# Performance work log

Hardware: AMD Instinct MI355X
Metric: run time of the kernel (lower is better)

Reference implementation:

```python
import jax, jax.numpy as jnp
import numpy as np

N_NODES = 100000
N_EDGES = 1600000
D_IN = 256
D_OUT = 128


def setup_inputs() -> dict:
    key = jax.random.key(0)
    k1, k2, k3, k4, k5, k6 = jax.random.split(key, 6)
    inp = {
        "input": jax.random.normal(k1, (N_NODES, D_IN), dtype=jnp.float32),
        "edge_row": jax.random.randint(k2, (N_EDGES,), 0, N_NODES),
        "edge_col": jax.random.randint(k3, (N_EDGES,), 0, N_NODES),
        "edge_val": jax.random.uniform(k4, (N_EDGES,), dtype=jnp.float32),
        "W": jax.random.normal(k5, (D_IN, D_OUT), dtype=jnp.float32) * (1.0 / np.sqrt(D_IN)),
        "b": jax.random.normal(k6, (D_OUT,), dtype=jnp.float32) * 0.01,
    }
    return inp


def reference(input, edge_row, edge_col, edge_val, W, b):
    # support = Linear(input)  -> [N, D_OUT]
    support = jnp.dot(input, W) + b
    # sparse.mm(adj, support): out[r] = sum_e val[e] * support[col[e]] for edges with row[e]==r
    msgs = edge_val[:, None] * support[edge_col]  # [E, D_OUT]
    agg = jax.ops.segment_sum(msgs, edge_row, num_segments=N_NODES)  # [N, D_OUT]
    return jnp.tanh(agg)
```

## Files before the change

### kernel.cpp

```cpp
#include <hip/hip_runtime.h>
#include <math.h>

#define N_NODES 100000
#define N_EDGES 1600000
#define D_IN 256
#define D_OUT 128

#define BN 64
#define BK 32

#define OFF_SUPPORT 0
#define OFF_COUNTS  51200000
#define OFF_CSREV   51600008
#define OFF_BSUMS   64400008

#define SCAN_CHUNK  1024
#define SCAN_BLOCKS ((N_NODES + SCAN_CHUNK - 1) / SCAN_CHUNK)

#define GEMM_BLOCKS ((N_NODES + BN - 1) / BN)
#define GEMM_SPLIT  860
#define EDGE_BLOCKS ((N_EDGES + 255) / 256)

__device__ __forceinline__ void gemm_body(
    int gb, const float* __restrict__ input, const float* __restrict__ W,
    const float* __restrict__ b, float* __restrict__ support) {
  __shared__ float As[BK][BN + 4];
  __shared__ float Ws[BK][D_OUT];

  const int t = threadIdx.x;
  const int node0 = gb * BN;
  const int fg = t & 31;
  const int ng = t >> 5;

  float acc[8][4];
#pragma unroll
  for (int i = 0; i < 8; i++)
#pragma unroll
    for (int j = 0; j < 4; j++) acc[i][j] = 0.f;

  for (int k0 = 0; k0 < D_IN; k0 += BK) {
#pragma unroll
    for (int j = 0; j < 2; j++) {
      int i = t + j * 256;
      int an = i >> 3;
      int ak = (i & 7) << 2;
      float4 v = make_float4(0.f, 0.f, 0.f, 0.f);
      if (node0 + an < N_NODES)
        v = *(const float4*)(input + (size_t)(node0 + an) * D_IN + k0 + ak);
      As[ak + 0][an] = v.x;
      As[ak + 1][an] = v.y;
      As[ak + 2][an] = v.z;
      As[ak + 3][an] = v.w;
    }
#pragma unroll
    for (int j = 0; j < 4; j++) {
      int i = t + j * 256;
      int wk = i >> 5;
      int wf = (i & 31) << 2;
      *(float4*)&Ws[wk][wf] = *(const float4*)(W + (size_t)(k0 + wk) * D_OUT + wf);
    }
    __syncthreads();

#pragma unroll 8
    for (int k = 0; k < BK; k++) {
      float4 w4 = *(const float4*)&Ws[k][fg << 2];
      float4 a0 = *(const float4*)&As[k][ng << 3];
      float4 a1 = *(const float4*)&As[k][(ng << 3) + 4];
      float a[8] = {a0.x, a0.y, a0.z, a0.w, a1.x, a1.y, a1.z, a1.w};
      float w[4] = {w4.x, w4.y, w4.z, w4.w};
#pragma unroll
      for (int i = 0; i < 8; i++)
#pragma unroll
        for (int j = 0; j < 4; j++)
          acc[i][j] = fmaf(a[i], w[j], acc[i][j]);
    }
    __syncthreads();
  }

  const float4 bv = *(const float4*)(b + (fg << 2));
#pragma unroll
  for (int i = 0; i < 8; i++) {
    int n = node0 + (ng << 3) + i;
    if (n < N_NODES) {
      float4 o;
      o.x = acc[i][0] + bv.x;
      o.y = acc[i][1] + bv.y;
      o.z = acc[i][2] + bv.z;
      o.w = acc[i][3] + bv.w;
      *(float4*)(support + (size_t)n * D_OUT + (fg << 2)) = o;
    }
  }
}

__global__ __launch_bounds__(256) void gemm_hist_kernel(
    const float* __restrict__ input, const float* __restrict__ W,
    const float* __restrict__ b, float* __restrict__ support,
    const int* __restrict__ erow, int* __restrict__ counts,
    int* __restrict__ pos_e) {
  if (blockIdx.x < GEMM_SPLIT) {
    gemm_body(blockIdx.x, input, W, b, support);
  } else {
    int e = (blockIdx.x - GEMM_SPLIT) * 256 + threadIdx.x;
    if (e < N_EDGES) pos_e[e] = atomicAdd(&counts[erow[e]], 1);
  }
}

__global__ __launch_bounds__(256) void gemm_build_kernel(
    const float* __restrict__ input, const float* __restrict__ W,
    const float* __restrict__ b, float* __restrict__ support,
    const int* __restrict__ erow, const int* __restrict__ ecol,
    const float* __restrict__ eval, const int* __restrict__ offsets,
    const int* __restrict__ pos_e, int2* __restrict__ csr_ev) {
  if (blockIdx.x < GEMM_BLOCKS - GEMM_SPLIT) {
    gemm_body(blockIdx.x + GEMM_SPLIT, input, W, b, support);
  } else {
    int e = (blockIdx.x - (GEMM_BLOCKS - GEMM_SPLIT)) * 256 + threadIdx.x;
    if (e < N_EDGES) {
      int idx = offsets[erow[e]] + pos_e[e];
      csr_ev[idx] = make_int2(ecol[e], __float_as_int(eval[e]));
    }
  }
}

__global__ __launch_bounds__(256) void scan_phase1(const int* __restrict__ counts,
                                                   int* __restrict__ bsums) {
  __shared__ int ts[256];
  int t = threadIdx.x;
  int idx0 = blockIdx.x * SCAN_CHUNK + t * 4;
  int s = 0;
#pragma unroll
  for (int i = 0; i < 4; i++)
    if (idx0 + i < N_NODES) s += counts[idx0 + i];
  ts[t] = s;
  __syncthreads();
#pragma unroll
  for (int off = 128; off > 0; off >>= 1) {
    if (t < off) ts[t] += ts[t + off];
    __syncthreads();
  }
  if (t == 0) bsums[blockIdx.x] = ts[0];
}

__global__ __launch_bounds__(128) void scan_phase2(int* __restrict__ bsums) {
  __shared__ int s[128];
  int t = threadIdx.x;
  int v = (t < SCAN_BLOCKS) ? bsums[t] : 0;
  s[t] = v;
  __syncthreads();
#pragma unroll
  for (int off = 1; off < 128; off <<= 1) {
    int x = (t >= off) ? s[t - off] : 0;
    __syncthreads();
    s[t] += x;
    __syncthreads();
  }
  if (t < SCAN_BLOCKS) bsums[t] = s[t] - v;
}

__global__ __launch_bounds__(256) void scan_phase3(int* __restrict__ counts,
                                                   const int* __restrict__ bsums) {
  __shared__ int ts[256];
  int t = threadIdx.x;
  int b = blockIdx.x;
  int idx0 = b * SCAN_CHUNK + t * 4;
  int v[4];
  int s = 0;
#pragma unroll
  for (int i = 0; i < 4; i++) {
    v[i] = (idx0 + i < N_NODES) ? counts[idx0 + i] : 0;
    s += v[i];
  }
  ts[t] = s;
  __syncthreads();
#pragma unroll
  for (int off = 1; off < 256; off <<= 1) {
    int x = (t >= off) ? ts[t - off] : 0;
    __syncthreads();
    ts[t] += x;
    __syncthreads();
  }
  int run = bsums[b] + ts[t] - s;
#pragma unroll
  for (int i = 0; i < 4; i++) {
    int idx = idx0 + i;
    if (idx < N_NODES) counts[idx] = run;
    run += v[i];
  }
  if (b == 0 && t == 0) counts[N_NODES] = N_EDGES;
}

__global__ __launch_bounds__(128) void agg_kernel(
    const int* __restrict__ offsets, const int2* __restrict__ csr_ev,
    const float* __restrict__ support, float* __restrict__ out) {
  int r = blockIdx.x;
  int f = threadIdx.x;
  int beg = offsets[r];
  int end = offsets[r + 1];
  float acc = 0.f;
  int j = beg;
  for (; j + 4 <= end; j += 4) {
    int2 e0 = csr_ev[j + 0];
    int2 e1 = csr_ev[j + 1];
    int2 e2 = csr_ev[j + 2];
    int2 e3 = csr_ev[j + 3];
    float s0 = support[(size_t)e0.x * D_OUT + f];
    float s1 = support[(size_t)e1.x * D_OUT + f];
    float s2 = support[(size_t)e2.x * D_OUT + f];
    float s3 = support[(size_t)e3.x * D_OUT + f];
    acc = fmaf(__int_as_float(e0.y), s0, acc);
    acc = fmaf(__int_as_float(e1.y), s1, acc);
    acc = fmaf(__int_as_float(e2.y), s2, acc);
    acc = fmaf(__int_as_float(e3.y), s3, acc);
  }
  for (; j < end; j++) {
    int2 ev = csr_ev[j];
    acc = fmaf(__int_as_float(ev.y), support[(size_t)ev.x * D_OUT + f], acc);
  }
  out[(size_t)r * D_OUT + f] = tanhf(acc);
}

extern "C" void kernel_launch(void* const* d_in, const int* in_sizes, int n_in,
                              void* d_out, int out_size, void* d_ws, size_t ws_size,
                              hipStream_t stream) {
  const float* input = (const float*)d_in[0];
  const int* erow = (const int*)d_in[1];
  const int* ecol = (const int*)d_in[2];
  const float* eval = (const float*)d_in[3];
  const float* W = (const float*)d_in[4];
  const float* b = (const float*)d_in[5];
  float* out = (float*)d_out;

  char* ws = (char*)d_ws;
  float* support = (float*)(ws + OFF_SUPPORT);
  int* counts = (int*)(ws + OFF_COUNTS);
  int2* csr_ev = (int2*)(ws + OFF_CSREV);
  int* bsums = (int*)(ws + OFF_BSUMS);
  int* pos_e = (int*)d_out;

  hipMemsetAsync(ws + OFF_COUNTS, 0, (size_t)(N_NODES + 1) * 4, stream);

  hipLaunchKernelGGL(gemm_hist_kernel, dim3(GEMM_SPLIT + EDGE_BLOCKS), dim3(256),
                     0, stream, input, W, b, support, erow, counts, pos_e);
  hipLaunchKernelGGL(scan_phase1, dim3(SCAN_BLOCKS), dim3(256), 0, stream,
                     counts, bsums);
  hipLaunchKernelGGL(scan_phase2, dim3(1), dim3(128), 0, stream, bsums);
  hipLaunchKernelGGL(scan_phase3, dim3(SCAN_BLOCKS), dim3(256), 0, stream,
                     counts, bsums);
  hipLaunchKernelGGL(gemm_build_kernel,
                     dim3((GEMM_BLOCKS - GEMM_SPLIT) + EDGE_BLOCKS), dim3(256),
                     0, stream, input, W, b, support, erow, ecol, eval, counts,
                     pos_e, csr_ev);
  hipLaunchKernelGGL(agg_kernel, dim3(N_NODES), dim3(128), 0, stream, counts,
                     csr_ev, support, out);
}
```

Baseline: 425.0 us.

## Move dense GEMM to bf16x3 split-precision MFMA with 128-row tiles

Replaces the scalar FP32 FMA GEMM with MFMA 16x16x32 bf16 instructions. Each FP32 value is split into hi and lo bf16 parts, and three products (hh, hl, lh) are accumulated to keep roughly FP32 accuracy. The tile grows to 128 nodes per block and the split point between the two fused kernels is adjusted to match. The cost is extra conversion work and LDS traffic, and the output stores are scalar and strided rather than float4.

```diff
diff --git a/kernel.cpp b/kernel.cpp
--- a/kernel.cpp
+++ b/kernel.cpp
@@ -6,9 +6,6 @@
 #define D_IN 256
 #define D_OUT 128
 
-#define BN 64
-#define BK 32
-
 #define OFF_SUPPORT 0
 #define OFF_COUNTS  51200000
 #define OFF_CSREV   51600008
@@ -17,77 +14,112 @@
 #define SCAN_CHUNK  1024
 #define SCAN_BLOCKS ((N_NODES + SCAN_CHUNK - 1) / SCAN_CHUNK)
 
-#define GEMM_BLOCKS ((N_NODES + BN - 1) / BN)
-#define GEMM_SPLIT  860
+#define GB 128
+#define GEMM_BLOCKS ((N_NODES + GB - 1) / GB)
+#define GEMM_SPLIT  391
 #define EDGE_BLOCKS ((N_EDGES + 255) / 256)
+
+#define AP 40
+
+typedef __attribute__((ext_vector_type(8))) short s8v;
+typedef __attribute__((ext_vector_type(4))) float f4v;
+
+__device__ __forceinline__ short f2bf(float x) {
+  unsigned u = __float_as_uint(x);
+  unsigned r = u + 0x7FFF + ((u >> 16) & 1);
+  return (short)(r >> 16);
+}
+__device__ __forceinline__ float bf2f(short h) {
+  return __uint_as_float(((unsigned)(unsigned short)h) << 16);
+}
 
 __device__ __forceinline__ void gemm_body(
     int gb, const float* __restrict__ input, const float* __restrict__ W,
     const float* __restrict__ b, float* __restrict__ support) {
-  __shared__ float As[BK][BN + 4];
-  __shared__ float Ws[BK][D_OUT];
+  __shared__ short Ahi[GB * AP];
+  __shared__ short Alo[GB * AP];
+  __shared__ short Bhi[D_OUT * AP];
+  __shared__ short Blo[D_OUT * AP];
 
   const int t = threadIdx.x;
-  const int node0 = gb * BN;
-  const int fg = t & 31;
-  const int ng = t >> 5;
-
-  float acc[8][4];
-#pragma unroll
-  for (int i = 0; i < 8; i++)
-#pragma unroll
-    for (int j = 0; j < 4; j++) acc[i][j] = 0.f;
-
-  for (int k0 = 0; k0 < D_IN; k0 += BK) {
-#pragma unroll
-    for (int j = 0; j < 2; j++) {
-      int i = t + j * 256;
-      int an = i >> 3;
-      int ak = (i & 7) << 2;
-      float4 v = make_float4(0.f, 0.f, 0.f, 0.f);
-      if (node0 + an < N_NODES)
-        v = *(const float4*)(input + (size_t)(node0 + an) * D_IN + k0 + ak);
-      As[ak + 0][an] = v.x;
-      As[ak + 1][an] = v.y;
-      As[ak + 2][an] = v.z;
-      As[ak + 3][an] = v.w;
-    }
+  const int node0 = gb * GB;
+  const int lane = t & 63;
+  const int wv = t >> 6;
+  const int qm = lane & 15;
+  const int quad = lane >> 4;
+
+  f4v acc[2][8];
+#pragma unroll
+  for (int mt = 0; mt < 2; mt++)
+#pragma unroll
+    for (int nt = 0; nt < 8; nt++) acc[mt][nt] = (f4v){0.f, 0.f, 0.f, 0.f};
+
+  for (int k0 = 0; k0 < D_IN; k0 += 32) {
 #pragma unroll
     for (int j = 0; j < 4; j++) {
       int i = t + j * 256;
-      int wk = i >> 5;
-      int wf = (i & 31) << 2;
-      *(float4*)&Ws[wk][wf] = *(const float4*)(W + (size_t)(k0 + wk) * D_OUT + wf);
-    }
-    __syncthreads();
-
-#pragma unroll 8
-    for (int k = 0; k < BK; k++) {
-      float4 w4 = *(const float4*)&Ws[k][fg << 2];
-      float4 a0 = *(const float4*)&As[k][ng << 3];
-      float4 a1 = *(const float4*)&As[k][(ng << 3) + 4];
-      float a[8] = {a0.x, a0.y, a0.z, a0.w, a1.x, a1.y, a1.z, a1.w};
-      float w[4] = {w4.x, w4.y, w4.z, w4.w};
-#pragma unroll
-      for (int i = 0; i < 8; i++)
-#pragma unroll
-        for (int j = 0; j < 4; j++)
-          acc[i][j] = fmaf(a[i], w[j], acc[i][j]);
-    }
-    __syncthreads();
-  }
-
-  const float4 bv = *(const float4*)(b + (fg << 2));
-#pragma unroll
-  for (int i = 0; i < 8; i++) {
-    int n = node0 + (ng << 3) + i;
-    if (n < N_NODES) {
-      float4 o;
-      o.x = acc[i][0] + bv.x;
-      o.y = acc[i][1] + bv.y;
-      o.z = acc[i][2] + bv.z;
-      o.w = acc[i][3] + bv.w;
-      *(float4*)(support + (size_t)n * D_OUT + (fg << 2)) = o;
+      int row = i >> 3;
+      int kf = (i & 7) << 2;
+      int node = node0 + row;
+      float4 v = make_float4(0.f, 0.f, 0.f, 0.f);
+      if (node < N_NODES)
+        v = *(const float4*)(input + (size_t)node * D_IN + k0 + kf);
+      short4 h, l;
+      h.x = f2bf(v.x); l.x = f2bf(v.x - bf2f(h.x));
+      h.y = f2bf(v.y); l.y = f2bf(v.y - bf2f(h.y));
+      h.z = f2bf(v.z); l.z = f2bf(v.z - bf2f(h.z));
+      h.w = f2bf(v.w); l.w = f2bf(v.w - bf2f(h.w));
+      *(short4*)&Ahi[row * AP + kf] = h;
+      *(short4*)&Alo[row * AP + kf] = l;
+    }
+#pragma unroll
+    for (int j = 0; j < 4; j++) {
+      int i = t + j * 256;
+      int kk = i >> 5;
+      int nf = (i & 31) << 2;
+      float4 v = *(const float4*)(W + (size_t)(k0 + kk) * D_OUT + nf);
+      float vv[4] = {v.x, v.y, v.z, v.w};
+#pragma unroll
+      for (int c = 0; c < 4; c++) {
+        short h = f2bf(vv[c]);
+        Bhi[(nf + c) * AP + kk] = h;
+        Blo[(nf + c) * AP + kk] = f2bf(vv[c] - bf2f(h));
+      }
+    }
+    __syncthreads();
+
+    s8v ah0 = *(s8v*)&Ahi[(wv * 32 + qm) * AP + quad * 8];
+    s8v al0 = *(s8v*)&Alo[(wv * 32 + qm) * AP + quad * 8];
+    s8v ah1 = *(s8v*)&Ahi[(wv * 32 + 16 + qm) * AP + quad * 8];
+    s8v al1 = *(s8v*)&Alo[(wv * 32 + 16 + qm) * AP + quad * 8];
+#pragma unroll
+    for (int nt = 0; nt < 8; nt++) {
+      s8v bh = *(s8v*)&Bhi[(nt * 16 + qm) * AP + quad * 8];
+      s8v bl = *(s8v*)&Blo[(nt * 16 + qm) * AP + quad * 8];
+      acc[0][nt] = __builtin_amdgcn_mfma_f32_16x16x32_bf16(ah0, bh, acc[0][nt], 0, 0, 0);
+      acc[0][nt] = __builtin_amdgcn_mfma_f32_16x16x32_bf16(ah0, bl, acc[0][nt], 0, 0, 0);
+      acc[0][nt] = __builtin_amdgcn_mfma_f32_16x16x32_bf16(al0, bh, acc[0][nt], 0, 0, 0);
+      acc[1][nt] = __builtin_amdgcn_mfma_f32_16x16x32_bf16(ah1, bh, acc[1][nt], 0, 0, 0);
+      acc[1][nt] = __builtin_amdgcn_mfma_f32_16x16x32_bf16(ah1, bl, acc[1][nt], 0, 0, 0);
+      acc[1][nt] = __builtin_amdgcn_mfma_f32_16x16x32_bf16(al1, bh, acc[1][nt], 0, 0, 0);
+    }
+    __syncthreads();
+  }
+
+  float bias[8];
+#pragma unroll
+  for (int nt = 0; nt < 8; nt++) bias[nt] = b[nt * 16 + qm];
+#pragma unroll
+  for (int mt = 0; mt < 2; mt++) {
+#pragma unroll
+    for (int nt = 0; nt < 8; nt++) {
+      int col = nt * 16 + qm;
+#pragma unroll
+      for (int r = 0; r < 4; r++) {
+        int node = node0 + wv * 32 + mt * 16 + quad * 4 + r;
+        if (node < N_NODES)
+          support[(size_t)node * D_OUT + col] = acc[mt][nt][r] + bias[nt];
+      }
     }
   }
 }
```

Measured after the change: 433.0 us. Within noise of the previous version (+1.9%).
